# Optimization experiments

Hardware: AMD Instinct MI355X
Metric: run time of the kernel (lower is better)

The kernel has to match this reference:

```python
import jax, jax.numpy as jnp
import numpy as np

N = 50000
E = 1600000
AUG = 6
IN = 128
HEADS = 8
HID = 16
OUT = 40


def setup_inputs() -> dict:
    key = jax.random.key(0)
    ks = jax.random.split(key, 14)
    s = 0.1
    return {
        "x": jax.random.normal(ks[0], (N, IN + AUG), jnp.float32),
        "edge_index": jax.random.randint(ks[1], (2, E), 0, N, jnp.int32),
        "mlp_w1": jax.random.normal(ks[2], (AUG, 16), jnp.float32) * s,
        "mlp_b1": jnp.zeros((16,), jnp.float32),
        "mlp_w2": jax.random.normal(ks[3], (16, 1), jnp.float32) * s,
        "mlp_b2": jnp.zeros((1,), jnp.float32),
        "w1": jax.random.normal(ks[4], (IN, HEADS * HID), jnp.float32) * s,
        "att_src1": jax.random.normal(ks[5], (HEADS, HID), jnp.float32) * s,
        "att_dst1": jax.random.normal(ks[6], (HEADS, HID), jnp.float32) * s,
        "bias1": jnp.zeros((HEADS * HID,), jnp.float32),
        "w2": jax.random.normal(ks[7], (HEADS * HID, OUT), jnp.float32) * s,
        "att_src2": jax.random.normal(ks[8], (1, OUT), jnp.float32) * s,
        "att_dst2": jax.random.normal(ks[9], (1, OUT), jnp.float32) * s,
        "bias2": jnp.zeros((OUT,), jnp.float32),
    }


def _gat_conv(x, src, dst, W, att_src, att_dst, bias, concat):
    # PyG GATConv (eval mode): linear -> per-edge leaky_relu attention ->
    # softmax over incoming edges per destination -> weighted scatter-sum.
    n = x.shape[0]
    heads, ch = att_src.shape
    h = (x @ W).reshape(n, heads, ch)                # [N,H,C]
    a_src = (h * att_src[None]).sum(-1)              # [N,H]
    a_dst = (h * att_dst[None]).sum(-1)              # [N,H]
    e = jax.nn.leaky_relu(a_src[src] + a_dst[dst], 0.2)  # [E,H]
    emax = jax.ops.segment_max(e, dst, num_segments=n)   # self-loops ensure nonempty
    p = jnp.exp(e - emax[dst])
    denom = jax.ops.segment_sum(p, dst, num_segments=n)
    alpha = p / denom[dst]                           # [E,H]
    msg = h[src] * alpha[:, :, None]                 # [E,H,C]
    out = jax.ops.segment_sum(msg, dst, num_segments=n)  # [N,H,C]
    out = out.reshape(n, heads * ch) if concat else out.mean(axis=1)
    return out + bias


def reference(x, edge_index, mlp_w1, mlp_b1, mlp_w2, mlp_b2,
              w1, att_src1, att_dst1, bias1, w2, att_src2, att_dst2, bias2):
    n = x.shape[0]
    orig = x[:, :-AUG]
    aug = x[:, -AUG:]
    aug = (aug - aug.mean(axis=0)) / jnp.std(aug, axis=0, ddof=1)  # torch std is unbiased
    scale = jax.nn.sigmoid(jax.nn.relu(aug @ mlp_w1 + mlp_b1) @ mlp_w2 + mlp_b2)  # [N,1]
    h = orig * (1.0 + scale)
    # dropout is identity in eval mode
    loops = jnp.arange(n, dtype=edge_index.dtype)
    src = jnp.concatenate([edge_index[0], loops])
    dst = jnp.concatenate([edge_index[1], loops])
    h = jax.nn.relu(_gat_conv(h, src, dst, w1, att_src1, att_dst1, bias1, True))
    out = _gat_conv(h, src, dst, w2, att_src2, att_dst2, bias2, False)
    return jax.nn.log_softmax(out, axis=1)
```

## Files before the change

kernel.cpp:

```cpp
#include <hip/hip_runtime.h>
#include <hip/hip_fp16.h>

#define XDIM 134
#define FEAT 128
#define AUGN 6
#define NH 8
#define HD 16
#define OUTD 40
#define PS 132
#define SB 256
#define PB 256
#define MAXNB 256
#define G8S 64
#define WTS 130
#define DST 132
#define W2C 48
#define DST2 52

typedef float v2f __attribute__((ext_vector_type(2)));
typedef _Float16 h8t __attribute__((ext_vector_type(8)));
typedef float f32x4 __attribute__((ext_vector_type(4)));

__device__ __forceinline__ float rlf(float v, int lane) {
  return __int_as_float(__builtin_amdgcn_readlane(__float_as_int(v), lane));
}

__global__ __launch_bounds__(256) void k_stats1(const float* __restrict__ x,
                                                float* __restrict__ part,
                                                int N) {
  __shared__ float red[4][12];
  float s[AUGN] = {0, 0, 0, 0, 0, 0}, q[AUGN] = {0, 0, 0, 0, 0, 0};
  for (int n = blockIdx.x * blockDim.x + threadIdx.x; n < N;
       n += gridDim.x * blockDim.x) {
    const float* r = x + (size_t)n * XDIM + FEAT;
    float2 v0 = *(const float2*)r;
    float2 v1 = *(const float2*)(r + 2);
    float2 v2 = *(const float2*)(r + 4);
    float v[AUGN] = {v0.x, v0.y, v1.x, v1.y, v2.x, v2.y};
#pragma unroll
    for (int i = 0; i < AUGN; i++) {
      s[i] += v[i];
      q[i] += v[i] * v[i];
    }
  }
#pragma unroll
  for (int i = 0; i < AUGN; i++) {
    for (int m = 1; m < 64; m <<= 1) {
      s[i] += __shfl_xor(s[i], m);
      q[i] += __shfl_xor(q[i], m);
    }
  }
  int wv = threadIdx.x >> 6, l = threadIdx.x & 63;
  if (l == 0) {
#pragma unroll
    for (int i = 0; i < AUGN; i++) {
      red[wv][i] = s[i];
      red[wv][6 + i] = q[i];
    }
  }
  __syncthreads();
  int t = threadIdx.x;
  if (t < 12) {
    part[blockIdx.x * 12 + t] =
        red[0][t] + red[1][t] + red[2][t] + red[3][t];
  }
}

__global__ __launch_bounds__(256) void k_scale(
    const float* __restrict__ x, const float* __restrict__ part,
    const float* __restrict__ w1, const float* __restrict__ b1,
    const float* __restrict__ w2, const float* __restrict__ b2,
    float* __restrict__ scl, int N) {
  __shared__ float red[4][12];
  __shared__ float sred[12];
  int t = threadIdx.x;
  {
    float v[12];
#pragma unroll
    for (int c = 0; c < 12; c++) v[c] = part[t * 12 + c];
#pragma unroll
    for (int c = 0; c < 12; c++)
      for (int m = 1; m < 64; m <<= 1) v[c] += __shfl_xor(v[c], m);
    int wv = t >> 6, l = t & 63;
    if (l == 0) {
#pragma unroll
      for (int c = 0; c < 12; c++) red[wv][c] = v[c];
    }
    __syncthreads();
    if (t < 12) sred[t] = red[0][t] + red[1][t] + red[2][t] + red[3][t];
    __syncthreads();
  }
  int n = blockIdx.x * 256 + t;
  if (n >= N) return;
  const float* r = x + (size_t)n * XDIM + FEAT;
  float a[AUGN];
  float invN = 1.0f / (float)N;
#pragma unroll
  for (int i = 0; i < AUGN; i++) {
    float sum = sred[i], sq = sred[6 + i];
    float mean = sum * invN;
    float var = (sq - sum * mean) / (float)(N - 1);
    a[i] = (r[i] - mean) / sqrtf(var);
  }
  float s2 = b2[0];
#pragma unroll
  for (int j = 0; j < 16; j++) {
    float z = b1[j];
#pragma unroll
    for (int i = 0; i < AUGN; i++) z = fmaf(a[i], w1[i * 16 + j], z);
    z = fmaxf(z, 0.0f);
    s2 = fmaf(z, w2[j], s2);
  }
  float sig = 1.0f / (1.0f + __expf(-s2));
  scl[n] = 1.0f + sig;
}

__global__ __launch_bounds__(256) void k_bh(const int* __restrict__ ei,
                                            int* __restrict__ cnt, int E,
                                            int NB) {
  __shared__ int hist[MAXNB];
  int t = threadIdx.x;
  for (int b = t; b < NB; b += 256) hist[b] = 0;
  __syncthreads();
  int ch = (E + PB - 1) / PB;
  int lo = blockIdx.x * ch, hi = min(lo + ch, E);
  for (int e = lo + t; e < hi; e += 256)
    atomicAdd(&hist[ei[E + e] >> 8], 1);
  __syncthreads();
  for (int b = t; b < NB; b += 256)
    cnt[(size_t)b * PB + blockIdx.x] = hist[b];
}

__global__ __launch_bounds__(256) void k_sc1(int* __restrict__ cnt,
                                             int* __restrict__ bsum) {
  __shared__ int ps[256];
  int b = blockIdx.x, t = threadIdx.x;
  int v = cnt[(size_t)b * PB + t];
  ps[t] = v;
  __syncthreads();
  for (int d = 1; d < 256; d <<= 1) {
    int u = (t >= d) ? ps[t - d] : 0;
    __syncthreads();
    ps[t] += u;
    __syncthreads();
  }
  cnt[(size_t)b * PB + t] = ps[t] - v;
  if (t == 255) bsum[b] = ps[255];
}

__global__ __launch_bounds__(256) void k_part(const int* __restrict__ ei,
                                              const int* __restrict__ cnt,
                                              const int* __restrict__ bsum,
                                              int* __restrict__ ebuf, int E,
                                              int NB) {
  __shared__ int bex[MAXNB];
  __shared__ int cur[MAXNB];
  int t = threadIdx.x;
  int v = (t < NB) ? bsum[t] : 0;
  bex[t] = v;
  __syncthreads();
  for (int d = 1; d < 256; d <<= 1) {
    int u = (t >= d) ? bex[t - d] : 0;
    __syncthreads();
    bex[t] += u;
    __syncthreads();
  }
  if (t < NB) cur[t] = (bex[t] - v) + cnt[(size_t)t * PB + blockIdx.x];
  __syncthreads();
  int ch = (E + PB - 1) / PB;
  int lo = blockIdx.x * ch, hi = min(lo + ch, E);
  for (int e = lo + t; e < hi; e += 256) {
    int s = ei[e], d = ei[E + e];
    int pos = atomicAdd(&cur[d >> 8], 1);
    ebuf[pos] = (s << 8) | (d & 255);
  }
}

__global__ __launch_bounds__(256) void k_bcsr(const int* __restrict__ ebuf,
                                              const int* __restrict__ bsum,
                                              int* __restrict__ offs,
                                              int* __restrict__ csr, int N,
                                              int E, int NB) {
  __shared__ int bex[MAXNB];
  __shared__ int dl[256];
  __shared__ int sc[256];
  __shared__ int cu[256];
  int b = blockIdx.x, t = threadIdx.x;
  {
    int v = (t < NB) ? bsum[t] : 0;
    bex[t] = v;
    __syncthreads();
    for (int d = 1; d < 256; d <<= 1) {
      int u = (t >= d) ? bex[t - d] : 0;
      __syncthreads();
      bex[t] += u;
      __syncthreads();
    }
    int incl = bex[t];
    __syncthreads();
    bex[t] = incl - v;
    __syncthreads();
  }
  int nn = min(256, N - b * 256);
  int rs = bex[b];
  int re = (b + 1 < NB) ? bex[b + 1] : E;
  int csrbase = rs + b * 256;
  dl[t] = 0;
  __syncthreads();
  for (int j = rs + t; j < re; j += 256)
    atomicAdd(&dl[ebuf[j] & 255], 1);
  __syncthreads();
  int v = (t < nn) ? dl[t] + 1 : 0;
  sc[t] = v;
  __syncthreads();
  for (int d = 1; d < 256; d <<= 1) {
    int u = (t >= d) ? sc[t - d] : 0;
    __syncthreads();
    sc[t] += u;
    __syncthreads();
  }
  int excl = sc[t] - v;
  if (t < nn) {
    int node = b * 256 + t;
    offs[node] = csrbase + excl;
    csr[csrbase + excl] = node;
    cu[t] = excl + 1;
  }
  __syncthreads();
  for (int j = rs + t; j < re; j += 256) {
    int pk = ebuf[j];
    int p = atomicAdd(&cu[pk & 255], 1);
    csr[csrbase + p] = pk >> 8;
  }
  if (b == 0 && t == 0) offs[N] = E + N;
}

__global__ __launch_bounds__(256) void k_gemm1(
    const float* __restrict__ x, const float* __restrict__ scl,
    const float* __restrict__ W, const float* __restrict__ asv,
    const float* __restrict__ adv, unsigned char* __restrict__ h8,
    float* __restrict__ a_src, float* __restrict__ a_dst, int N) {
  __shared__ __half WT[128 * WTS];
  __shared__ __half D16[64 * DST];
  int tid = threadIdx.x;
  int wv = tid >> 6, l = tid & 63;
  int q = l >> 4, c = l & 15;
  for (int idx = tid; idx < 128 * 128; idx += 256) {
    int k = idx >> 7, n = idx & 127;
    WT[n * WTS + k] = __float2half(W[idx]);
  }
  __syncthreads();
  int colBase = wv * 32;
  h8t bf[2][4];
  const unsigned short* wtp = (const unsigned short*)WT;
#pragma unroll
  for (int ct = 0; ct < 2; ct++) {
#pragma unroll
    for (int kk = 0; kk < 4; kk++) {
      unsigned int* bu = (unsigned int*)&bf[ct][kk];
      int base = (colBase + ct * 16 + c) * WTS + kk * 32 + 8 * q;
#pragma unroll
      for (int p = 0; p < 4; p++)
        bu[p] = *(const unsigned int*)(wtp + base + 2 * p);
    }
  }
  int nodeBase = blockIdx.x * 64;
#pragma unroll
  for (int nt = 0; nt < 4; nt++) {
    int node = nodeBase + nt * 16 + c;
    const float* xr = x + (size_t)min(node, N - 1) * XDIM;
    h8t af[4];
#pragma unroll
    for (int kk = 0; kk < 4; kk++) {
      int k0 = kk * 32 + 8 * q;
#pragma unroll
      for (int p = 0; p < 4; p++) {
        float2 v = *(const float2*)(xr + k0 + 2 * p);
        af[kk][2 * p] = (_Float16)v.x;
        af[kk][2 * p + 1] = (_Float16)v.y;
      }
    }
    f32x4 a0 = {0.f, 0.f, 0.f, 0.f}, a1 = {0.f, 0.f, 0.f, 0.f};
#pragma unroll
    for (int kk = 0; kk < 4; kk++) {
      a0 = __builtin_amdgcn_mfma_f32_16x16x32_f16(af[kk], bf[0][kk], a0, 0, 0, 0);
      a1 = __builtin_amdgcn_mfma_f32_16x16x32_f16(af[kk], bf[1][kk], a1, 0, 0, 0);
    }
#pragma unroll
    for (int r = 0; r < 4; r++) {
      int row = nt * 16 + 4 * q + r;
      D16[row * DST + colBase + c] = __float2half(a0[r]);
      D16[row * DST + colBase + 16 + c] = __float2half(a1[r]);
    }
  }
  __syncthreads();
  float asw0 = asv[2 * l], asw1 = asv[2 * l + 1];
  float adw0 = adv[2 * l], adw1 = adv[2 * l + 1];
  for (int i = 0; i < 16; i++) {
    int node = nodeBase + wv * 16 + i;
    if (node >= N) break;
    float s = scl[node];
    __half2 yh = *(const __half2*)&D16[(wv * 16 + i) * DST + 2 * l];
    float2 yf = __half22float2(yh);
    float y0 = yf.x * s, y1 = yf.y * s;
    int pk = __builtin_amdgcn_cvt_pk_fp8_f32(y0, y1, 0, false);
    ((unsigned short*)(h8 + (size_t)node * FEAT))[l] = (unsigned short)pk;
    float ps = y0 * asw0 + y1 * asw1;
    float pd = y0 * adw0 + y1 * adw1;
    ps += __shfl_xor(ps, 1); ps += __shfl_xor(ps, 2); ps += __shfl_xor(ps, 4);
    pd += __shfl_xor(pd, 1); pd += __shfl_xor(pd, 2); pd += __shfl_xor(pd, 4);
    if ((l & 7) == 0) {
      a_src[node * NH + (l >> 3)] = ps;
      a_dst[node * NH + (l >> 3)] = pd;
    }
  }
}

__global__ __launch_bounds__(256) void k_agg1(
    const int* __restrict__ offs, const int* __restrict__ csr,
    const float* __restrict__ a_src, const float* __restrict__ a_dst,
    const unsigned char* __restrict__ h8, const float* __restrict__ bias,
    __half* __restrict__ h2h, int N) {
  __shared__ float plds[4][8 * PS];
  __shared__ int slds[4][128];
  int wv = threadIdx.x >> 6, l = threadIdx.x & 63;
  int n = blockIdx.x * 4 + wv;
  if (n >= N) return;
  int beg = offs[n], end = offs[n + 1];
  int deg = end - beg;
  int h = l & 7, e8 = l >> 3;
  float adh = a_dst[(size_t)n * NH + h];
  float smh = 0.0f;
  for (int j0 = 0; j0 < deg; j0 += 8) {
    int j = j0 + e8;
    if (j < deg) {
      int s = csr[beg + j];
      if (h == 0 && j < 128) slds[wv][j] = s;
      float t = a_src[(size_t)s * NH + h] + adh;
      t = t > 0.0f ? t : 0.2f * t;
      float p = __expf(t);
      smh += p;
      if (j < 128) plds[wv][h * PS + j] = p;
    }
  }
  smh += __shfl_xor(smh, 8);
  smh += __shfl_xor(smh, 16);
  smh += __shfl_xor(smh, 32);
  __builtin_amdgcn_wave_barrier();
  int li = l & 15, eg = l >> 4;
  int hh = li >> 1;
  float rd = 1.0f / __shfl(smh, hh);
  const int* sp = slds[wv];
  const float* pp = &plds[wv][hh * PS];
  float acc0 = 0.f, acc1 = 0.f, acc2 = 0.f, acc3 = 0.f;
  float acc4 = 0.f, acc5 = 0.f, acc6 = 0.f, acc7 = 0.f;
  if (deg <= 128) {
    int dm1 = deg - 1;
    int ns = (deg + 3) >> 2;
    uint2 A[4], B[4];
#define ROWA(G) \
  (*(const uint2*)(h8 + (size_t)sp[min(4 * (G) + eg, dm1)] * FEAT + 8 * li))
#pragma unroll
    for (int i = 0; i < 4; i++) A[i] = ROWA(i);
#pragma unroll
    for (int i = 0; i < 4; i++) B[i] = ROWA(4 + i);
    for (int g = 0; g < ns; g += 4) {
#pragma unroll
      for (int i = 0; i < 4; i++) {
        uint2 w = A[i];
        A[i] = B[i];
        B[i] = ROWA(g + 8 + i);
        int j = 4 * (g + i) + eg;
        float a = (j < deg) ? pp[j] : 0.0f;
        v2f l0 = __builtin_amdgcn_cvt_pk_f32_fp8((int)w.x, false);
        v2f h0 = __builtin_amdgcn_cvt_pk_f32_fp8((int)w.x, true);
        v2f l1 = __builtin_amdgcn_cvt_pk_f32_fp8((int)w.y, false);
        v2f h1 = __builtin_amdgcn_cvt_pk_f32_fp8((int)w.y, true);
        acc0 = fmaf(a, l0[0], acc0); acc1 = fmaf(a, l0[1], acc1);
        acc2 = fmaf(a, h0[0], acc2); acc3 = fmaf(a, h0[1], acc3);
        acc4 = fmaf(a, l1[0], acc4); acc5 = fmaf(a, l1[1], acc5);
        acc6 = fmaf(a, h1[0], acc6); acc7 = fmaf(a, h1[1], acc7);
      }
    }
#undef ROWA
  } else {
    float adhh = __shfl(adh, hh);
    for (int j = eg; j < deg; j += 4) {
      int s;
      float p;
      if (j < 128) {
        s = sp[j];
        p = pp[j];
      } else {
        s = csr[beg + j];
        float t = a_src[(size_t)s * NH + hh] + adhh;
        t = t > 0.0f ? t : 0.2f * t;
        p = __expf(t);
      }
      uint2 w = *(const uint2*)(h8 + (size_t)s * FEAT + 8 * li);
      v2f l0 = __builtin_amdgcn_cvt_pk_f32_fp8((int)w.x, false);
      v2f h0 = __builtin_amdgcn_cvt_pk_f32_fp8((int)w.x, true);
      v2f l1 = __builtin_amdgcn_cvt_pk_f32_fp8((int)w.y, false);
      v2f h1 = __builtin_amdgcn_cvt_pk_f32_fp8((int)w.y, true);
      acc0 = fmaf(p, l0[0], acc0); acc1 = fmaf(p, l0[1], acc1);
      acc2 = fmaf(p, h0[0], acc2); acc3 = fmaf(p, h0[1], acc3);
      acc4 = fmaf(p, l1[0], acc4); acc5 = fmaf(p, l1[1], acc5);
      acc6 = fmaf(p, h1[0], acc6); acc7 = fmaf(p, h1[1], acc7);
    }
  }
#pragma unroll
  for (int m = 16; m < 64; m <<= 1) {
    acc0 += __shfl_xor(acc0, m); acc1 += __shfl_xor(acc1, m);
    acc2 += __shfl_xor(acc2, m); acc3 += __shfl_xor(acc3, m);
    acc4 += __shfl_xor(acc4, m); acc5 += __shfl_xor(acc5, m);
    acc6 += __shfl_xor(acc6, m); acc7 += __shfl_xor(acc7, m);
  }
  if (l < 16) {
    float4 b0 = *(const float4*)(bias + 8 * l);
    float4 b1v = *(const float4*)(bias + 8 * l + 4);
    float o0 = fmaxf(acc0 * rd + b0.x, 0.0f);
    float o1 = fmaxf(acc1 * rd + b0.y, 0.0f);
    float o2 = fmaxf(acc2 * rd + b0.z, 0.0f);
    float o3 = fmaxf(acc3 * rd + b0.w, 0.0f);
    float o4 = fmaxf(acc4 * rd + b1v.x, 0.0f);
    float o5 = fmaxf(acc5 * rd + b1v.y, 0.0f);
    float o6 = fmaxf(acc6 * rd + b1v.z, 0.0f);
    float o7 = fmaxf(acc7 * rd + b1v.w, 0.0f);
    __half2 pa = __float22half2_rn(make_float2(o0, o1));
    __half2 pb = __float22half2_rn(make_float2(o2, o3));
    __half2 pc = __float22half2_rn(make_float2(o4, o5));
    __half2 pd2 = __float22half2_rn(make_float2(o6, o7));
    uint4 st;
    st.x = *(unsigned int*)&pa;
    st.y = *(unsigned int*)&pb;
    st.z = *(unsigned int*)&pc;
    st.w = *(unsigned int*)&pd2;
    *(uint4*)(h2h + (size_t)n * FEAT + 8 * l) = st;
  }
}

__global__ __launch_bounds__(256) void k_gemm2(
    const __half* __restrict__ h2h, const float* __restrict__ W,
    const float* __restrict__ asv, const float* __restrict__ adv,
    unsigned char* __restrict__ g8, float* __restrict__ a_src,
    float* __restrict__ a_dst, int N) {
  __shared__ __half WT2[W2C * WTS];
  __shared__ float DL[64 * DST2];
  int tid = threadIdx.x;
  int wv = tid >> 6, l = tid & 63;
  int q = l >> 4, c = l & 15;
  for (int idx = tid; idx < W2C * 128; idx += 256) {
    int col = idx >> 7, k = idx & 127;
    float v = (col < OUTD) ? W[k * OUTD + col] : 0.0f;
    WT2[col * WTS + k] = __float2half(v);
  }
  __syncthreads();
  h8t bf[3][4];
  const unsigned short* wtp = (const unsigned short*)WT2;
#pragma unroll
  for (int ct = 0; ct < 3; ct++) {
#pragma unroll
    for (int kk = 0; kk < 4; kk++) {
      unsigned int* bu = (unsigned int*)&bf[ct][kk];
      int base = (ct * 16 + c) * WTS + kk * 32 + 8 * q;
#pragma unroll
      for (int p = 0; p < 4; p++)
        bu[p] = *(const unsigned int*)(wtp + base + 2 * p);
    }
  }
  int nodeBase = blockIdx.x * 64;
  int node = nodeBase + wv * 16 + c;
  const __half* hr = h2h + (size_t)min(node, N - 1) * FEAT;
  h8t af[4];
#pragma unroll
  for (int kk = 0; kk < 4; kk++) {
    uint4 v = *(const uint4*)(hr + kk * 32 + 8 * q);
    *(uint4*)&af[kk] = v;
  }
  f32x4 d0 = {0.f, 0.f, 0.f, 0.f}, d1 = {0.f, 0.f, 0.f, 0.f},
        d2 = {0.f, 0.f, 0.f, 0.f};
#pragma unroll
  for (int kk = 0; kk < 4; kk++) {
    d0 = __builtin_amdgcn_mfma_f32_16x16x32_f16(af[kk], bf[0][kk], d0, 0, 0, 0);
    d1 = __builtin_amdgcn_mfma_f32_16x16x32_f16(af[kk], bf[1][kk], d1, 0, 0, 0);
    d2 = __builtin_amdgcn_mfma_f32_16x16x32_f16(af[kk], bf[2][kk], d2, 0, 0, 0);
  }
#pragma unroll
  for (int r = 0; r < 4; r++) {
    int row = wv * 16 + 4 * q + r;
    DL[row * DST2 + c] = d0[r];
    DL[row * DST2 + 16 + c] = d1[r];
    DL[row * DST2 + 32 + c] = d2[r];
  }
  __syncthreads();
  int i = l & 15, cg = l >> 4;
  int row = wv * 16 + i;
  float ps = 0.0f, pd = 0.0f;
#pragma unroll
  for (int k = 0; k < 10; k++) {
    int col = cg * 10 + k;
    float gv = DL[row * DST2 + col];
    ps = fmaf(gv, asv[col], ps);
    pd = fmaf(gv, adv[col], pd);
  }
  ps += __shfl_xor(ps, 16); ps += __shfl_xor(ps, 32);
  pd += __shfl_xor(pd, 16); pd += __shfl_xor(pd, 32);
  int snode = nodeBase + wv * 16 + i;
  if (cg == 0 && snode < N) {
    a_src[snode] = ps;
    a_dst[snode] = pd;
  }
  for (int idx = l; idx < 16 * 16; idx += 64) {
    int ni = idx >> 4, w = idx & 15;
    int rr = wv * 16 + ni;
    int wnode = nodeBase + rr;
    if (wnode < N) {
      unsigned int u = 0;
      if (w < 10) {
        float c0 = DL[rr * DST2 + 4 * w];
        float c1 = DL[rr * DST2 + 4 * w + 1];
        float c2 = DL[rr * DST2 + 4 * w + 2];
        float c3 = DL[rr * DST2 + 4 * w + 3];
        u = __builtin_amdgcn_cvt_pk_fp8_f32(c0, c1, 0, false);
        u = __builtin_amdgcn_cvt_pk_fp8_f32(c2, c3, u, true);
      }
      *(unsigned int*)(g8 + (size_t)wnode * G8S + 4 * w) = u;
    }
  }
}

__global__ __launch_bounds__(256) void k_agg2(
    const int* __restrict__ offs, const int* __restrict__ csr,
    const float* __restrict__ a_src, const float* __restrict__ a_dst,
    const unsigned char* __restrict__ g8, const float* __restrict__ bias,
    float* __restrict__ out, int N) {
  __shared__ float plds[4][PS];
  __shared__ int slds[4][128];
  int wv = threadIdx.x >> 6, l = threadIdx.x & 63;
  int n = blockIdx.x * 4 + wv;
  if (n >= N) return;
  int beg = offs[n], end = offs[n + 1];
  int deg = end - beg;
  float adn = a_dst[n];
  float sm = 0.0f;
  for (int j0 = 0; j0 < deg; j0 += 64) {
    int j = j0 + l;
    if (j < deg) {
      int s = csr[beg + j];
      float t = a_src[s] + adn;
      t = t > 0.0f ? t : 0.2f * t;
      float p = __expf(t);
      sm += p;
      if (j < 128) {
        plds[wv][j] = p;
        slds[wv][j] = s;
      }
    }
  }
  for (int m = 1; m < 64; m <<= 1) sm += __shfl_xor(sm, m);
  float rd = 1.0f / sm;
  const int* sp = slds[wv];
  const float* pp = plds[wv];
  int li = l & 15, eg = l >> 4;
  int lic = min(li, 9);
  const unsigned char* gb = g8 + 4 * lic;
  float acc0 = 0.0f, acc1 = 0.0f, acc2 = 0.0f, acc3 = 0.0f;
  if (deg <= 128) {
    int dm1 = deg - 1;
    int ns = (deg + 3) >> 2;
    unsigned int cur[4], nxt[4];
#define ROWB(G) \
  (*(const unsigned int*)(gb + (size_t)sp[min(4 * (G) + eg, dm1)] * G8S))
#pragma unroll
    for (int i = 0; i < 4; i++) cur[i] = ROWB(i);
    for (int g = 0; g < ns; g += 4) {
#pragma unroll
      for (int i = 0; i < 4; i++) nxt[i] = ROWB(g + 4 + i);
#pragma unroll
      for (int i = 0; i < 4; i++) {
        int j = 4 * (g + i) + eg;
        float a = (j < deg) ? pp[j] : 0.0f;
        v2f lo = __builtin_amdgcn_cvt_pk_f32_fp8((int)cur[i], false);
        v2f hi = __builtin_amdgcn_cvt_pk_f32_fp8((int)cur[i], true);
        acc0 = fmaf(a, lo[0], acc0);
        acc1 = fmaf(a, lo[1], acc1);
        acc2 = fmaf(a, hi[0], acc2);
        acc3 = fmaf(a, hi[1], acc3);
        cur[i] = nxt[i];
      }
    }
#undef ROWB
  } else {
    for (int j = eg; j < deg; j += 4) {
      int s;
      float p;
      if (j < 128) {
        s = sp[j];
        p = pp[j];
      } else {
        s = csr[beg + j];
        float t = a_src[s] + adn;
        t = t > 0.0f ? t : 0.2f * t;
        p = __expf(t);
      }
      unsigned int w = *(const unsigned int*)(gb + (size_t)s * G8S);
      v2f lo = __builtin_amdgcn_cvt_pk_f32_fp8((int)w, false);
      v2f hi = __builtin_amdgcn_cvt_pk_f32_fp8((int)w, true);
      acc0 = fmaf(p, lo[0], acc0);
      acc1 = fmaf(p, lo[1], acc1);
      acc2 = fmaf(p, hi[0], acc2);
      acc3 = fmaf(p, hi[1], acc3);
    }
  }
#pragma unroll
  for (int m = 16; m < 64; m <<= 1) {
    acc0 += __shfl_xor(acc0, m);
    acc1 += __shfl_xor(acc1, m);
    acc2 += __shfl_xor(acc2, m);
    acc3 += __shfl_xor(acc3, m);
  }
  bool cact = li < 10;
  float v0 = -INFINITY, v1 = -INFINITY, v2 = -INFINITY, v3 = -INFINITY;
  if (cact) {
    float4 bv = *(const float4*)(bias + 4 * li);
    v0 = acc0 * rd + bv.x;
    v1 = acc1 * rd + bv.y;
    v2 = acc2 * rd + bv.z;
    v3 = acc3 * rd + bv.w;
  }
  float mx = fmaxf(fmaxf(v0, v1), fmaxf(v2, v3));
  for (int m = 1; m < 64; m <<= 1) mx = fmaxf(mx, __shfl_xor(mx, m));
  float pe = (eg == 0 && cact) ? __expf(v0 - mx) + __expf(v1 - mx) +
                                     __expf(v2 - mx) + __expf(v3 - mx)
                               : 0.0f;
  float se = pe;
  for (int m = 1; m < 64; m <<= 1) se += __shfl_xor(se, m);
  float ls = logf(se);
  if (eg == 0 && cact) {
    float4 o;
    o.x = v0 - mx - ls;
    o.y = v1 - mx - ls;
    o.z = v2 - mx - ls;
    o.w = v3 - mx - ls;
    *(float4*)(out + (size_t)n * OUTD + 4 * li) = o;
  }
}

extern "C" void kernel_launch(void* const* d_in, const int* in_sizes, int n_in,
                              void* d_out, int out_size, void* d_ws,
                              size_t ws_size, hipStream_t stream) {
  const float* x = (const float*)d_in[0];
  const int* ei = (const int*)d_in[1];
  const float* mw1 = (const float*)d_in[2];
  const float* mb1 = (const float*)d_in[3];
  const float* mw2 = (const float*)d_in[4];
  const float* mb2 = (const float*)d_in[5];
  const float* W1 = (const float*)d_in[6];
  const float* as1w = (const float*)d_in[7];
  const float* ad1w = (const float*)d_in[8];
  const float* b1 = (const float*)d_in[9];
  const float* W2 = (const float*)d_in[10];
  const float* as2w = (const float*)d_in[11];
  const float* ad2w = (const float*)d_in[12];
  const float* b2 = (const float*)d_in[13];
  float* out = (float*)d_out;

  int N = in_sizes[0] / XDIM;
  int E = in_sizes[1] / 2;
  int ET = E + N;
  int NB = (N + 255) >> 8;

  char* ws = (char*)d_ws;
  size_t off = 0;
  auto carve = [&](size_t bytes) -> void* {
    void* p = ws + off;
    off = (off + bytes + 255) & ~(size_t)255;
    return p;
  };
  float* part = (float*)carve((size_t)SB * 12 * 4);
  int* cnt = (int*)carve((size_t)NB * PB * 4);
  int* bsum = (int*)carve((size_t)MAXNB * 4);
  int* ebuf = (int*)carve((size_t)E * 4);
  int* offs = (int*)carve((size_t)(N + 1) * 4);
  int* csr = (int*)carve((size_t)ET * 4);
  float* scl = (float*)carve((size_t)N * 4);
  float* as1 = (float*)carve((size_t)N * NH * 4);
  float* ad1 = (float*)carve((size_t)N * NH * 4);
  unsigned char* h8 = (unsigned char*)carve((size_t)N * FEAT);
  __half* h2h = (__half*)carve((size_t)N * FEAT * 2);
  unsigned char* g8 = (unsigned char*)carve((size_t)N * G8S);
  float* as2 = (float*)carve((size_t)N * 4);
  float* ad2 = (float*)carve((size_t)N * 4);

  k_stats1<<<SB, 256, 0, stream>>>(x, part, N);
  k_scale<<<(N + 255) / 256, 256, 0, stream>>>(x, part, mw1, mb1, mw2, mb2,
                                               scl, N);
  k_bh<<<PB, 256, 0, stream>>>(ei, cnt, E, NB);
  k_sc1<<<NB, 256, 0, stream>>>(cnt, bsum);
  k_part<<<PB, 256, 0, stream>>>(ei, cnt, bsum, ebuf, E, NB);
  k_bcsr<<<NB, 256, 0, stream>>>(ebuf, bsum, offs, csr, N, E, NB);
  int NG = (N + 63) / 64;
  k_gemm1<<<NG, 256, 0, stream>>>(x, scl, W1, as1w, ad1w, h8, as1, ad1, N);
  k_agg1<<<(N + 3) / 4, 256, 0, stream>>>(offs, csr, as1, ad1, h8, b1, h2h, N);
  k_gemm2<<<NG, 256, 0, stream>>>(h2h, W2, as2w, ad2w, g8, as2, ad2, N);
  k_agg2<<<(N + 3) / 4, 256, 0, stream>>>(offs, csr, as2, ad2, g8, b2, out, N);
}
```

Baseline: 184.6 us.

## Store layer-1 attention logits in fp16 and restructure agg1 prefetch

Layer-1 per-node attention source and destination scores are stored as half precision, which halves the bytes of the random per-edge a_src gathers in the aggregation kernel. The W1 transpose load in gemm1 now reads float4 vectors. The agg1 row-prefetch pipeline changes from a two-deep rolling buffer loaded per element to a one-group-ahead batch prefetch, which shortens how far ahead loads are issued. Rounding the attention logits to fp16 adds small errors to the softmax weights.

```diff
diff --git a/kernel.cpp b/kernel.cpp
--- a/kernel.cpp
+++ b/kernel.cpp
@@ -239,15 +239,19 @@
     const float* __restrict__ x, const float* __restrict__ scl,
     const float* __restrict__ W, const float* __restrict__ asv,
     const float* __restrict__ adv, unsigned char* __restrict__ h8,
-    float* __restrict__ a_src, float* __restrict__ a_dst, int N) {
+    __half* __restrict__ as1h, __half* __restrict__ ad1h, int N) {
   __shared__ __half WT[128 * WTS];
   __shared__ __half D16[64 * DST];
   int tid = threadIdx.x;
   int wv = tid >> 6, l = tid & 63;
   int q = l >> 4, c = l & 15;
-  for (int idx = tid; idx < 128 * 128; idx += 256) {
+  for (int idx = tid * 4; idx < 128 * 128; idx += 256 * 4) {
     int k = idx >> 7, n = idx & 127;
-    WT[n * WTS + k] = __float2half(W[idx]);
+    float4 v = *(const float4*)(W + idx);
+    WT[(n + 0) * WTS + k] = __float2half(v.x);
+    WT[(n + 1) * WTS + k] = __float2half(v.y);
+    WT[(n + 2) * WTS + k] = __float2half(v.z);
+    WT[(n + 3) * WTS + k] = __float2half(v.w);
   }
   __syncthreads();
   int colBase = wv * 32;
@@ -310,15 +314,15 @@
     ps += __shfl_xor(ps, 1); ps += __shfl_xor(ps, 2); ps += __shfl_xor(ps, 4);
     pd += __shfl_xor(pd, 1); pd += __shfl_xor(pd, 2); pd += __shfl_xor(pd, 4);
     if ((l & 7) == 0) {
-      a_src[node * NH + (l >> 3)] = ps;
-      a_dst[node * NH + (l >> 3)] = pd;
+      as1h[node * NH + (l >> 3)] = __float2half(ps);
+      ad1h[node * NH + (l >> 3)] = __float2half(pd);
     }
   }
 }
 
 __global__ __launch_bounds__(256) void k_agg1(
     const int* __restrict__ offs, const int* __restrict__ csr,
-    const float* __restrict__ a_src, const float* __restrict__ a_dst,
+    const __half* __restrict__ as1h, const __half* __restrict__ ad1h,
     const unsigned char* __restrict__ h8, const float* __restrict__ bias,
     __half* __restrict__ h2h, int N) {
   __shared__ float plds[4][8 * PS];
@@ -329,14 +333,14 @@
   int beg = offs[n], end = offs[n + 1];
   int deg = end - beg;
   int h = l & 7, e8 = l >> 3;
-  float adh = a_dst[(size_t)n * NH + h];
+  float adh = __half2float(ad1h[(size_t)n * NH + h]);
   float smh = 0.0f;
   for (int j0 = 0; j0 < deg; j0 += 8) {
     int j = j0 + e8;
     if (j < deg) {
       int s = csr[beg + j];
       if (h == 0 && j < 128) slds[wv][j] = s;
-      float t = a_src[(size_t)s * NH + h] + adh;
+      float t = __half2float(as1h[(size_t)s * NH + h]) + adh;
       t = t > 0.0f ? t : 0.2f * t;
       float p = __expf(t);
       smh += p;
@@ -357,29 +361,27 @@
   if (deg <= 128) {
     int dm1 = deg - 1;
     int ns = (deg + 3) >> 2;
-    uint2 A[4], B[4];
+    uint2 cur[4], nxt[4];
 #define ROWA(G) \
   (*(const uint2*)(h8 + (size_t)sp[min(4 * (G) + eg, dm1)] * FEAT + 8 * li))
 #pragma unroll
-    for (int i = 0; i < 4; i++) A[i] = ROWA(i);
-#pragma unroll
-    for (int i = 0; i < 4; i++) B[i] = ROWA(4 + i);
+    for (int i = 0; i < 4; i++) cur[i] = ROWA(i);
     for (int g = 0; g < ns; g += 4) {
 #pragma unroll
+      for (int i = 0; i < 4; i++) nxt[i] = ROWA(g + 4 + i);
+#pragma unroll
       for (int i = 0; i < 4; i++) {
-        uint2 w = A[i];
-        A[i] = B[i];
-        B[i] = ROWA(g + 8 + i);
         int j = 4 * (g + i) + eg;
         float a = (j < deg) ? pp[j] : 0.0f;
-        v2f l0 = __builtin_amdgcn_cvt_pk_f32_fp8((int)w.x, false);
-        v2f h0 = __builtin_amdgcn_cvt_pk_f32_fp8((int)w.x, true);
-        v2f l1 = __builtin_amdgcn_cvt_pk_f32_fp8((int)w.y, false);
-        v2f h1 = __builtin_amdgcn_cvt_pk_f32_fp8((int)w.y, true);
+        v2f l0 = __builtin_amdgcn_cvt_pk_f32_fp8((int)cur[i].x, false);
+        v2f h0 = __builtin_amdgcn_cvt_pk_f32_fp8((int)cur[i].x, true);
+        v2f l1 = __builtin_amdgcn_cvt_pk_f32_fp8((int)cur[i].y, false);
+        v2f h1 = __builtin_amdgcn_cvt_pk_f32_fp8((int)cur[i].y, true);
         acc0 = fmaf(a, l0[0], acc0); acc1 = fmaf(a, l0[1], acc1);
         acc2 = fmaf(a, h0[0], acc2); acc3 = fmaf(a, h0[1], acc3);
         acc4 = fmaf(a, l1[0], acc4); acc5 = fmaf(a, l1[1], acc5);
         acc6 = fmaf(a, h1[0], acc6); acc7 = fmaf(a, h1[1], acc7);
+        cur[i] = nxt[i];
       }
     }
 #undef ROWA
@@ -393,7 +395,7 @@
         p = pp[j];
       } else {
         s = csr[beg + j];
-        float t = a_src[(size_t)s * NH + hh] + adhh;
+        float t = __half2float(as1h[(size_t)s * NH + hh]) + adhh;
         t = t > 0.0f ? t : 0.2f * t;
         p = __expf(t);
       }
@@ -684,8 +686,8 @@
   int* offs = (int*)carve((size_t)(N + 1) * 4);
   int* csr = (int*)carve((size_t)ET * 4);
   float* scl = (float*)carve((size_t)N * 4);
-  float* as1 = (float*)carve((size_t)N * NH * 4);
-  float* ad1 = (float*)carve((size_t)N * NH * 4);
+  __half* as1h = (__half*)carve((size_t)N * NH * 2);
+  __half* ad1h = (__half*)carve((size_t)N * NH * 2);
   unsigned char* h8 = (unsigned char*)carve((size_t)N * FEAT);
   __half* h2h = (__half*)carve((size_t)N * FEAT * 2);
   unsigned char* g8 = (unsigned char*)carve((size_t)N * G8S);
@@ -700,8 +702,9 @@
   k_part<<<PB, 256, 0, stream>>>(ei, cnt, bsum, ebuf, E, NB);
   k_bcsr<<<NB, 256, 0, stream>>>(ebuf, bsum, offs, csr, N, E, NB);
   int NG = (N + 63) / 64;
-  k_gemm1<<<NG, 256, 0, stream>>>(x, scl, W1, as1w, ad1w, h8, as1, ad1, N);
-  k_agg1<<<(N + 3) / 4, 256, 0, stream>>>(offs, csr, as1, ad1, h8, b1, h2h, N);
+  k_gemm1<<<NG, 256, 0, stream>>>(x, scl, W1, as1w, ad1w, h8, as1h, ad1h, N);
+  k_agg1<<<(N + 3) / 4, 256, 0, stream>>>(offs, csr, as1h, ad1h, h8, b1, h2h,
+                                          N);
   k_gemm2<<<NG, 256, 0, stream>>>(h2h, W2, as2w, ad2w, g8, as2, ad2, N);
   k_agg2<<<(N + 3) / 4, 256, 0, stream>>>(offs, csr, as2, ad2, g8, b2, out, N);
 }
```

Result: no change. 182.2 us (-1.3%).
